# Optimization experiments

Hardware: AMD Instinct MI355X
Metric: run time of the kernel (lower is better)

Reference implementation:

```python
import jax, jax.numpy as jnp
import numpy as np

EPS = 1e-12  # matches tf l2_normalize epsilon behavior closely enough for testing

def setup_inputs() -> dict:
    key = jax.random.key(0)
    k1, k2 = jax.random.split(key)
    B, M, D = 512, 65536, 512
    context = jax.random.normal(k1, (B, D), dtype=jnp.float32)
    memory = jax.random.normal(k2, (M, D), dtype=jnp.float32)
    return {"context": context, "memory": memory}

def reference(context, memory):
    # tf.keras.losses.cosine_similarity returns NEGATIVE cosine similarity:
    # sim[b,m] = -sum(l2norm(context[b]) * l2norm(memory[m]))
    ctx_n = context / jnp.sqrt(jnp.maximum(jnp.sum(context * context, axis=-1, keepdims=True), EPS))
    mem_n = memory / jnp.sqrt(jnp.maximum(jnp.sum(memory * memory, axis=-1, keepdims=True), EPS))
    sim = -jnp.einsum('bd,md->bm', ctx_n, mem_n)  # [B, M]
    best = jnp.argmin(sim, axis=-1)               # [B], = argmax cosine
    # recall: gather then expand_dims(axis=0) -> [1, B, D]
    return memory[best][None, :, :]
```

## Files before the change

kernel.cpp:

```cpp
#include <hip/hip_runtime.h>
#include <hip/hip_bf16.h>
#include <stdint.h>

#define D_DIM 512
#define B_CTX 512
#define M_MEM 65536
#define BM 128
#define BB 128
#define BK 32
#define GBK 64
#define LDSPAD 40
#define DELTA_COS 2.5e-3f
#define LISTCAP 2048
#define CVT_MEM_BLOCKS (M_MEM / 32)
#define CVT_BLOCKS (CVT_MEM_BLOCKS + B_CTX / 32)

typedef __attribute__((ext_vector_type(8))) short short8;
typedef __attribute__((ext_vector_type(4))) float floatx4;

__device__ __forceinline__ uint32_t f32_order(float s) {
    uint32_t u = __float_as_uint(s);
    return (u & 0x80000000u) ? ~u : (u | 0x80000000u);
}
__device__ __forceinline__ float f32_unorder(uint32_t v) {
    uint32_t u = (v & 0x80000000u) ? (v & 0x7FFFFFFFu) : ~v;
    return __uint_as_float(u);
}
__device__ __forceinline__ uint32_t pack_bf16_rtn(float a, float b) {
    uint32_t ua = __float_as_uint(a) + 0x8000u;
    uint32_t ub = __float_as_uint(b) + 0x8000u;
    return (ua >> 16) | (ub & 0xFFFF0000u);
}

typedef const __attribute__((address_space(1))) void gv_t;
typedef __attribute__((address_space(3))) void lv_t;
__device__ __forceinline__ void gload_lds16(const uint16_t* g, uint16_t* l) {
    __builtin_amdgcn_global_load_lds((gv_t*)g, (lv_t*)l, 16, 0, 0);
}

__global__ void detect_init(const uint32_t* __restrict__ mem_raw,
                            uint32_t* __restrict__ flag) {
    __shared__ int cnt;
    if (threadIdx.x == 0) cnt = 0;
    __syncthreads();
    int s = 0;
    #pragma unroll
    for (int i = 0; i < 8; ++i) {
        uint32_t u = mem_raw[threadIdx.x * 8 + i];
        uint32_t e = (u >> 7) & 0xFFu;
        s += (e >= 96u && e <= 144u) ? 1 : 0;
    }
    atomicAdd(&cnt, s);
    __syncthreads();
    if (threadIdx.x == 0) *flag = (cnt > 256) ? 1u : 0u;
}

__global__ __launch_bounds__(256) void convert_scale(const void* __restrict__ ctxv,
                                                     const void* __restrict__ memv,
                                                     const uint32_t* __restrict__ flag,
                                                     uint16_t* __restrict__ mem_s,
                                                     uint16_t* __restrict__ ctx_b) {
    const bool isbf = (*flag != 0u);
    const int lane = threadIdx.x & 63;
    const int w = threadIdx.x >> 6;
    if (blockIdx.x < CVT_MEM_BLOCKS) {
        const int gw = blockIdx.x * 4 + w;
        #pragma unroll
        for (int i = 0; i < 8; ++i) {
            const int r = gw * 8 + i;
            float x[8];
            if (isbf) {
                uint4 v = *((const uint4*)((const uint16_t*)memv + (size_t)r * D_DIM) + lane);
                uint32_t ww[4] = {v.x, v.y, v.z, v.w};
                #pragma unroll
                for (int j = 0; j < 4; ++j) {
                    x[2 * j]     = __uint_as_float(ww[j] << 16);
                    x[2 * j + 1] = __uint_as_float(ww[j] & 0xFFFF0000u);
                }
            } else {
                const float4* p = (const float4*)((const float*)memv + (size_t)r * D_DIM) + lane * 2;
                float4 a = p[0], bq = p[1];
                x[0] = a.x; x[1] = a.y; x[2] = a.z; x[3] = a.w;
                x[4] = bq.x; x[5] = bq.y; x[6] = bq.z; x[7] = bq.w;
            }
            float nsq = 0.f;
            #pragma unroll
            for (int j = 0; j < 8; ++j) nsq = fmaf(x[j], x[j], nsq);
            #pragma unroll
            for (int o = 32; o; o >>= 1) nsq += __shfl_xor(nsq, o, 64);
            const float invn = rsqrtf(fmaxf(nsq, 1e-12f));
            uint4 ov;
            ov.x = pack_bf16_rtn(x[0] * invn, x[1] * invn);
            ov.y = pack_bf16_rtn(x[2] * invn, x[3] * invn);
            ov.z = pack_bf16_rtn(x[4] * invn, x[5] * invn);
            ov.w = pack_bf16_rtn(x[6] * invn, x[7] * invn);
            *((uint4*)(mem_s + (size_t)r * D_DIM) + lane) = ov;
        }
    } else {
        const int gw = (blockIdx.x - CVT_MEM_BLOCKS) * 4 + w;
        #pragma unroll
        for (int i = 0; i < 8; ++i) {
            const int r = gw * 8 + i;
            uint4 ov;
            if (isbf) {
                ov = *((const uint4*)((const uint16_t*)ctxv + (size_t)r * D_DIM) + lane);
            } else {
                const float4* p = (const float4*)((const float*)ctxv + (size_t)r * D_DIM) + lane * 2;
                float4 a = p[0], bq = p[1];
                ov.x = pack_bf16_rtn(a.x, a.y);
                ov.y = pack_bf16_rtn(a.z, a.w);
                ov.z = pack_bf16_rtn(bq.x, bq.y);
                ov.w = pack_bf16_rtn(bq.z, bq.w);
            }
            *((uint4*)(ctx_b + (size_t)r * D_DIM) + lane) = ov;
        }
    }
}

__global__ __launch_bounds__(256) void score_mfma(const uint16_t* __restrict__ A,
                                                  const uint16_t* __restrict__ Bc,
                                                  uint32_t* __restrict__ tmax,
                                                  int coarse) {
    __shared__ __align__(16) uint16_t at[BM][GBK];
    __shared__ __align__(16) uint16_t bt[BB][GBK];
    __shared__ uint32_t s_gbest[8][BB];

    const int t    = threadIdx.x;
    const int b0   = blockIdx.x * BB;
    const int m0   = blockIdx.y * BM;
    const int lane = t & 63;
    const int w    = t >> 6;
    const int wm   = w >> 1;
    const int wb   = w & 1;
    const int quad = lane >> 4;
    const int l15  = lane & 15;
    const int srow = t >> 3;
    const int scol = (t & 7) * 8;

    floatx4 acc[4][4];
    #pragma unroll
    for (int i = 0; i < 4; ++i)
        #pragma unroll
        for (int j = 0; j < 4; ++j)
            acc[i][j] = (floatx4){0.f, 0.f, 0.f, 0.f};

    for (int k0 = 0; k0 < D_DIM; k0 += GBK) {
        __syncthreads();
        #pragma unroll
        for (int q = 0; q < 4; ++q) {
            const int r = srow + q * 32;
            gload_lds16(A  + (size_t)(m0 + r) * D_DIM + k0 + scol,
                        &at[0][0] + (size_t)(q * 256 + (w << 6)) * 8);
            gload_lds16(Bc + (size_t)(b0 + r) * D_DIM + k0 + scol,
                        &bt[0][0] + (size_t)(q * 256 + (w << 6)) * 8);
        }
        __syncthreads();
        #pragma unroll
        for (int kk = 0; kk < 2; ++kk) {
            short8 af[4], bg[4];
            #pragma unroll
            for (int i = 0; i < 4; ++i)
                af[i] = *(const short8*)&at[wm * 64 + i * 16 + l15][kk * 32 + quad * 8];
            #pragma unroll
            for (int j = 0; j < 4; ++j)
                bg[j] = *(const short8*)&bt[wb * 64 + j * 16 + l15][kk * 32 + quad * 8];
            #pragma unroll
            for (int i = 0; i < 4; ++i)
                #pragma unroll
                for (int j = 0; j < 4; ++j)
                    acc[i][j] = __builtin_amdgcn_mfma_f32_16x16x32_bf16(af[i], bg[j], acc[i][j], 0, 0, 0);
        }
    }

    #pragma unroll
    for (int i = 0; i < 4; ++i)
        #pragma unroll
        for (int j = 0; j < 4; ++j) {
            uint32_t k = 0;
            #pragma unroll
            for (int r = 0; r < 4; ++r) {
                uint32_t kk = f32_order(acc[i][j][r]);
                k = kk > k ? kk : k;
            }
            uint32_t o1 = __shfl_xor(k, 16, 64); k = o1 > k ? o1 : k;
            uint32_t o2 = __shfl_xor(k, 32, 64); k = o2 > k ? o2 : k;
            if (quad == 0) s_gbest[wm * 4 + i][wb * 64 + j * 16 + l15] = k;
        }
    __syncthreads();

    if (!coarse) {
        const int G0 = blockIdx.y * 8;
        for (int e = t; e < 8 * BB; e += 256) {
            const int col = e >> 3, g = e & 7;
            tmax[(size_t)(b0 + col) * 4096 + G0 + g] = s_gbest[g][col];
        }
    } else {
        if (t < BB) {
            uint32_t k = s_gbest[0][t];
            #pragma unroll
            for (int g = 1; g < 8; ++g) k = s_gbest[g][t] > k ? s_gbest[g][t] : k;
            tmax[(size_t)(b0 + t) * 512 + blockIdx.y] = k;
        }
    }
}

__global__ __launch_bounds__(256) void score_phase1(const void* __restrict__ ctxv,
                                                    const void* __restrict__ memv,
                                                    const uint32_t* __restrict__ flag,
                                                    uint32_t* __restrict__ tmax,
                                                    int coarse) {
    __shared__ __align__(16) uint16_t at[BM][LDSPAD];
    __shared__ __align__(16) uint16_t bt[BB][LDSPAD];
    __shared__ float s_nsq[BM];
    __shared__ uint32_t s_gbest[8][BB];

    const int t    = threadIdx.x;
    const int b0   = blockIdx.x * BB;
    const int m0   = blockIdx.y * BM;
    const int lane = t & 63;
    const int w    = t >> 6;
    const int wm   = w >> 1;
    const int wb   = w & 1;
    const int quad = lane >> 4;
    const int l15  = lane & 15;
    const int srow = t >> 2;
    const int scol = (t & 3) * 8;

    floatx4 acc[4][4];
    #pragma unroll
    for (int i = 0; i < 4; ++i)
        #pragma unroll
        for (int j = 0; j < 4; ++j)
            acc[i][j] = (floatx4){0.f, 0.f, 0.f, 0.f};

    float nsq0 = 0.f, nsq1 = 0.f;
    const bool isbf = (*flag != 0u);

    for (int k0 = 0; k0 < D_DIM; k0 += BK) {
        __syncthreads();
        if (isbf) {
            const uint16_t* mp = (const uint16_t*)memv;
            const uint16_t* cp = (const uint16_t*)ctxv;
            uint4 va0 = *(const uint4*)(mp + (size_t)(m0 + srow) * D_DIM + k0 + scol);
            uint4 va1 = *(const uint4*)(mp + (size_t)(m0 + srow + 64) * D_DIM + k0 + scol);
            uint4 vb0 = *(const uint4*)(cp + (size_t)(b0 + srow) * D_DIM + k0 + scol);
            uint4 vb1 = *(const uint4*)(cp + (size_t)(b0 + srow + 64) * D_DIM + k0 + scol);
            *(uint4*)&at[srow][scol] = va0;
            *(uint4*)&at[srow + 64][scol] = va1;
            *(uint4*)&bt[srow][scol] = vb0;
            *(uint4*)&bt[srow + 64][scol] = vb1;
            uint32_t wa0[4] = {va0.x, va0.y, va0.z, va0.w};
            uint32_t wa1[4] = {va1.x, va1.y, va1.z, va1.w};
            #pragma unroll
            for (int i = 0; i < 4; ++i) {
                float a = __uint_as_float(wa0[i] << 16);
                float b = __uint_as_float(wa0[i] & 0xFFFF0000u);
                nsq0 = fmaf(a, a, nsq0); nsq0 = fmaf(b, b, nsq0);
                float c = __uint_as_float(wa1[i] << 16);
                float d = __uint_as_float(wa1[i] & 0xFFFF0000u);
                nsq1 = fmaf(c, c, nsq1); nsq1 = fmaf(d, d, nsq1);
            }
        } else {
            const float* mp = (const float*)memv;
            const float* cp = (const float*)ctxv;
            const float4* pa0 = (const float4*)(mp + (size_t)(m0 + srow) * D_DIM + k0 + scol);
            const float4* pa1 = (const float4*)(mp + (size_t)(m0 + srow + 64) * D_DIM + k0 + scol);
            const float4* pb0 = (const float4*)(cp + (size_t)(b0 + srow) * D_DIM + k0 + scol);
            const float4* pb1 = (const float4*)(cp + (size_t)(b0 + srow + 64) * D_DIM + k0 + scol);
            float4 a0 = pa0[0], a1 = pa0[1], a2 = pa1[0], a3 = pa1[1];
            float4 c0 = pb0[0], c1 = pb0[1], c2 = pb1[0], c3 = pb1[1];
            uint4 va0 = {pack_bf16_rtn(a0.x, a0.y), pack_bf16_rtn(a0.z, a0.w),
                         pack_bf16_rtn(a1.x, a1.y), pack_bf16_rtn(a1.z, a1.w)};
            uint4 va1 = {pack_bf16_rtn(a2.x, a2.y), pack_bf16_rtn(a2.z, a2.w),
                         pack_bf16_rtn(a3.x, a3.y), pack_bf16_rtn(a3.z, a3.w)};
            uint4 vb0 = {pack_bf16_rtn(c0.x, c0.y), pack_bf16_rtn(c0.z, c0.w),
                         pack_bf16_rtn(c1.x, c1.y), pack_bf16_rtn(c1.z, c1.w)};
            uint4 vb1 = {pack_bf16_rtn(c2.x, c2.y), pack_bf16_rtn(c2.z, c2.w),
                         pack_bf16_rtn(c3.x, c3.y), pack_bf16_rtn(c3.z, c3.w)};
            *(uint4*)&at[srow][scol] = va0;
            *(uint4*)&at[srow + 64][scol] = va1;
            *(uint4*)&bt[srow][scol] = vb0;
            *(uint4*)&bt[srow + 64][scol] = vb1;
            nsq0 = fmaf(a0.x, a0.x, nsq0); nsq0 = fmaf(a0.y, a0.y, nsq0);
            nsq0 = fmaf(a0.z, a0.z, nsq0); nsq0 = fmaf(a0.w, a0.w, nsq0);
            nsq0 = fmaf(a1.x, a1.x, nsq0); nsq0 = fmaf(a1.y, a1.y, nsq0);
            nsq0 = fmaf(a1.z, a1.z, nsq0); nsq0 = fmaf(a1.w, a1.w, nsq0);
            nsq1 = fmaf(a2.x, a2.x, nsq1); nsq1 = fmaf(a2.y, a2.y, nsq1);
            nsq1 = fmaf(a2.z, a2.z, nsq1); nsq1 = fmaf(a2.w, a2.w, nsq1);
            nsq1 = fmaf(a3.x, a3.x, nsq1); nsq1 = fmaf(a3.y, a3.y, nsq1);
            nsq1 = fmaf(a3.z, a3.z, nsq1); nsq1 = fmaf(a3.w, a3.w, nsq1);
        }
        __syncthreads();

        short8 af[4], bg[4];
        #pragma unroll
        for (int i = 0; i < 4; ++i)
            af[i] = *(const short8*)&at[wm * 64 + i * 16 + l15][quad * 8];
        #pragma unroll
        for (int j = 0; j < 4; ++j)
            bg[j] = *(const short8*)&bt[wb * 64 + j * 16 + l15][quad * 8];

        #pragma unroll
        for (int i = 0; i < 4; ++i)
            #pragma unroll
            for (int j = 0; j < 4; ++j)
                acc[i][j] = __builtin_amdgcn_mfma_f32_16x16x32_bf16(af[i], bg[j], acc[i][j], 0, 0, 0);
    }

    nsq0 += __shfl_xor(nsq0, 1, 64); nsq0 += __shfl_xor(nsq0, 2, 64);
    nsq1 += __shfl_xor(nsq1, 1, 64); nsq1 += __shfl_xor(nsq1, 2, 64);
    __syncthreads();
    if ((t & 3) == 0) { s_nsq[srow] = nsq0; s_nsq[srow + 64] = nsq1; }
    __syncthreads();

    float invn[4][4];
    #pragma unroll
    for (int i = 0; i < 4; ++i)
        #pragma unroll
        for (int r = 0; r < 4; ++r)
            invn[i][r] = rsqrtf(fmaxf(s_nsq[wm * 64 + i * 16 + quad * 4 + r], 1e-12f));

    #pragma unroll
    for (int i = 0; i < 4; ++i)
        #pragma unroll
        for (int j = 0; j < 4; ++j) {
            uint32_t k = 0;
            #pragma unroll
            for (int r = 0; r < 4; ++r) {
                uint32_t kk = f32_order(acc[i][j][r] * invn[i][r]);
                k = kk > k ? kk : k;
            }
            uint32_t o1 = __shfl_xor(k, 16, 64); k = o1 > k ? o1 : k;
            uint32_t o2 = __shfl_xor(k, 32, 64); k = o2 > k ? o2 : k;
            if (quad == 0) s_gbest[wm * 4 + i][wb * 64 + j * 16 + l15] = k;
        }
    __syncthreads();

    if (!coarse) {
        const int G0 = blockIdx.y * 8;
        for (int e = t; e < 8 * BB; e += 256) {
            const int col = e >> 3, g = e & 7;
            tmax[(size_t)(b0 + col) * 4096 + G0 + g] = s_gbest[g][col];
        }
    } else {
        if (t < BB) {
            uint32_t k = s_gbest[0][t];
            #pragma unroll
            for (int g = 1; g < 8; ++g) k = s_gbest[g][t] > k ? s_gbest[g][t] : k;
            tmax[(size_t)(b0 + t) * 512 + blockIdx.y] = k;
        }
    }
}

__global__ __launch_bounds__(256) void phase2(const void* __restrict__ ctxv,
                                              const void* __restrict__ memv,
                                              const uint32_t* __restrict__ flag,
                                              const uint32_t* __restrict__ tmax,
                                              void* __restrict__ outv,
                                              int ngrp, int gshift) {
    __shared__ float s_ctx[D_DIM];
    __shared__ int s_list[LISTCAP];
    __shared__ int s_cnt;
    __shared__ uint32_t s_red[4];
    __shared__ float s_cn[4];
    __shared__ double s_d[4], s_n[4];
    __shared__ int s_m[4];
    __shared__ int s_bestm;

    const int b = blockIdx.x;
    const int t = threadIdx.x;
    const int lane = t & 63;
    const int w = t >> 6;
    const bool isbf = (*flag != 0u);
    const int gmask = (1 << gshift) - 1;

    if (t == 0) s_cnt = 0;
    if (isbf) {
        if (t < 64) {
            uint4 v = *((const uint4*)((const uint16_t*)ctxv + (size_t)b * D_DIM) + t);
            uint32_t ww[4] = {v.x, v.y, v.z, v.w};
            #pragma unroll
            for (int i = 0; i < 4; ++i) {
                s_ctx[t * 8 + 2 * i]     = __uint_as_float(ww[i] << 16);
                s_ctx[t * 8 + 2 * i + 1] = __uint_as_float(ww[i] & 0xFFFF0000u);
            }
        }
    } else {
        if (t < 128)
            ((float4*)s_ctx)[t] = ((const float4*)((const float*)ctxv + (size_t)b * D_DIM))[t];
    }
    __syncthreads();

    float cs = s_ctx[t] * s_ctx[t] + s_ctx[t + 256] * s_ctx[t + 256];
    #pragma unroll
    for (int o = 32; o; o >>= 1) cs += __shfl_xor(cs, o, 64);
    if (lane == 0) s_cn[w] = cs;

    const uint32_t* tk = tmax + (size_t)b * ngrp;
    const int nk = ngrp >> 8;
    uint32_t km = 0;
    for (int i = 0; i < nk; ++i) {
        uint32_t v = tk[t + (i << 8)];
        km = v > km ? v : km;
    }
    #pragma unroll
    for (int o = 32; o; o >>= 1) { uint32_t ot = __shfl_xor(km, o, 64); km = ot > km ? ot : km; }
    if (lane == 0) s_red[w] = km;
    __syncthreads();
    uint32_t kbest = s_red[0];
    #pragma unroll
    for (int i = 1; i < 4; ++i) kbest = s_red[i] > kbest ? s_red[i] : kbest;
    const float cnorm = sqrtf(s_cn[0] + s_cn[1] + s_cn[2] + s_cn[3]);
    const uint32_t keyT = f32_order(f32_unorder(kbest) - DELTA_COS * cnorm);

    for (int i = 0; i < nk; ++i) {
        uint32_t v = tk[t + (i << 8)];
        if (v >= keyT) {
            int idx = atomicAdd(&s_cnt, 1);
            if (idx < LISTCAP) s_list[idx] = t + (i << 8);
        }
    }
    __syncthreads();
    int cnt = s_cnt; if (cnt > LISTCAP) cnt = LISTCAP;
    const int total = cnt << gshift;

    double bd = -1.0e300, bn = 1.0;
    double bp = bd * 1.0e300;
    int bm = 0x7FFFFFFF;
    const float* cb = s_ctx + lane * 8;

    for (int base = w * 2; base < total; base += 8) {
        const bool has1 = (base + 1 < total);
        const int ia = base, ib = has1 ? base + 1 : base;
        const int ma = (s_list[ia >> gshift] << gshift) + (ia & gmask);
        const int mb = (s_list[ib >> gshift] << gshift) + (ib & gmask);
        double d0 = 0.0, n0 = 0.0, d1 = 0.0, n1 = 0.0;
        if (isbf) {
            uint4 va = *((const uint4*)((const uint16_t*)memv + (size_t)ma * D_DIM) + lane);
            uint4 vb = *((const uint4*)((const uint16_t*)memv + (size_t)mb * D_DIM) + lane);
            uint32_t wa[4] = {va.x, va.y, va.z, va.w};
            uint32_t wbv[4] = {vb.x, vb.y, vb.z, vb.w};
            #pragma unroll
            for (int i = 0; i < 4; ++i) {
                float a0 = __uint_as_float(wa[i] << 16);
                float a1 = __uint_as_float(wa[i] & 0xFFFF0000u);
                d0 += (double)a0 * (double)cb[2 * i];
                d0 += (double)a1 * (double)cb[2 * i + 1];
                n0 += (double)a0 * (double)a0 + (double)a1 * (double)a1;
                float b0v = __uint_as_float(wbv[i] << 16);
                float b1v = __uint_as_float(wbv[i] & 0xFFFF0000u);
                d1 += (double)b0v * (double)cb[2 * i];
                d1 += (double)b1v * (double)cb[2 * i + 1];
                n1 += (double)b0v * (double)b0v + (double)b1v * (double)b1v;
            }
        } else {
            const float4* pa = (const float4*)((const float*)memv + (size_t)ma * D_DIM) + lane * 2;
            const float4* pb = (const float4*)((const float*)memv + (size_t)mb * D_DIM) + lane * 2;
            float4 a0 = pa[0], a1 = pa[1], b0v = pb[0], b1v = pb[1];
            float xa[8] = {a0.x, a0.y, a0.z, a0.w, a1.x, a1.y, a1.z, a1.w};
            float xb[8] = {b0v.x, b0v.y, b0v.z, b0v.w, b1v.x, b1v.y, b1v.z, b1v.w};
            #pragma unroll
            for (int i = 0; i < 8; ++i) {
                d0 += (double)xa[i] * (double)cb[i];
                n0 += (double)xa[i] * (double)xa[i];
                d1 += (double)xb[i] * (double)cb[i];
                n1 += (double)xb[i] * (double)xb[i];
            }
        }
        #pragma unroll
        for (int o = 32; o; o >>= 1) {
            d0 += __shfl_xor(d0, o, 64);
            n0 += __shfl_xor(n0, o, 64);
            d1 += __shfl_xor(d1, o, 64);
            n1 += __shfl_xor(n1, o, 64);
        }
        double p0 = d0 * fabs(d0);
        double lhs = p0 * bn, rhs = bp * n0;
        if (lhs > rhs || (lhs == rhs && ma < bm)) { bd = d0; bn = n0; bp = p0; bm = ma; }
        if (has1) {
            double p1 = d1 * fabs(d1);
            double lhs1 = p1 * bn, rhs1 = bp * n1;
            if (lhs1 > rhs1 || (lhs1 == rhs1 && mb < bm)) { bd = d1; bn = n1; bp = p1; bm = mb; }
        }
    }
    if (lane == 0) { s_d[w] = bd; s_n[w] = bn; s_m[w] = bm; }
    __syncthreads();
    if (t == 0) {
        double cd = s_d[0], cn2 = s_n[0], cp = cd * fabs(cd);
        int cm = s_m[0];
        #pragma unroll
        for (int i = 1; i < 4; ++i) {
            double pd = s_d[i], pn = s_n[i], pp = pd * fabs(pd);
            double lhs = pp * cn2, rhs = cp * pn;
            if (lhs > rhs || (lhs == rhs && s_m[i] < cm)) { cd = pd; cn2 = pn; cp = pp; cm = s_m[i]; }
        }
        s_bestm = cm;
    }
    __syncthreads();
    const int mbest = s_bestm;
    if (isbf) {
        if (t < 64)
            ((uint4*)((uint16_t*)outv + (size_t)b * D_DIM))[t] =
                ((const uint4*)((const uint16_t*)memv + (size_t)mbest * D_DIM))[t];
    } else {
        if (t < 128)
            ((float4*)((float*)outv + (size_t)b * D_DIM))[t] =
                ((const float4*)((const float*)memv + (size_t)mbest * D_DIM))[t];
    }
}

extern "C" void kernel_launch(void* const* d_in, const int* in_sizes, int n_in,
                              void* d_out, int out_size, void* d_ws, size_t ws_size,
                              hipStream_t stream) {
    const void* ctx = d_in[0];
    const void* mem = d_in[1];
    if (in_sizes[0] > in_sizes[1]) { ctx = d_in[1]; mem = d_in[0]; }

    const size_t fineBytes   = (size_t)B_CTX * 4096 * 4;
    const size_t coarseBytes = (size_t)B_CTX * 512 * 4;
    const size_t ctxBytes    = (size_t)B_CTX * D_DIM * 2;
    const size_t memBytes    = (size_t)M_MEM * D_DIM * 2;
    const size_t fastBytes   = fineBytes + 256 + ctxBytes + memBytes;
    dim3 grid(B_CTX / BB, M_MEM / BM);

    if (ws_size >= fastBytes) {
        uint32_t* tmax  = (uint32_t*)d_ws;
        uint32_t* flag  = (uint32_t*)((char*)d_ws + fineBytes);
        uint16_t* ctx_b = (uint16_t*)((char*)d_ws + fineBytes + 256);
        uint16_t* mem_s = (uint16_t*)((char*)d_ws + fineBytes + 256 + ctxBytes);
        detect_init<<<1, 64, 0, stream>>>((const uint32_t*)mem, flag);
        convert_scale<<<CVT_BLOCKS, 256, 0, stream>>>(ctx, mem, flag, mem_s, ctx_b);
        score_mfma<<<grid, 256, 0, stream>>>(mem_s, ctx_b, tmax, 0);
        phase2<<<B_CTX, 256, 0, stream>>>(ctx, mem, flag, tmax, d_out, 4096, 4);
    } else if (ws_size >= fineBytes + 256) {
        uint32_t* tmax = (uint32_t*)d_ws;
        uint32_t* flag = (uint32_t*)((char*)d_ws + fineBytes);
        detect_init<<<1, 64, 0, stream>>>((const uint32_t*)mem, flag);
        score_phase1<<<grid, 256, 0, stream>>>(ctx, mem, flag, tmax, 0);
        phase2<<<B_CTX, 256, 0, stream>>>(ctx, mem, flag, tmax, d_out, 4096, 4);
    } else {
        uint32_t* tmax = (uint32_t*)d_ws;
        uint32_t* flag = (uint32_t*)((char*)d_ws + coarseBytes);
        detect_init<<<1, 64, 0, stream>>>((const uint32_t*)mem, flag);
        score_phase1<<<grid, 256, 0, stream>>>(ctx, mem, flag, tmax, 1);
        phase2<<<B_CTX, 256, 0, stream>>>(ctx, mem, flag, tmax, d_out, 512, 7);
    }
}
```

Baseline: 293.5 us.

## Double-buffer score_mfma LDS tiles with swizzled layout and remapped block order

```diff
diff --git a/kernel.cpp b/kernel.cpp
--- a/kernel.cpp
+++ b/kernel.cpp
@@ -8,7 +8,7 @@
 #define BM 128
 #define BB 128
 #define BK 32
-#define GBK 64
+#define GBK 32
 #define LDSPAD 40
 #define DELTA_COS 2.5e-3f
 #define LISTCAP 2048
@@ -117,25 +117,44 @@
     }
 }
 
-__global__ __launch_bounds__(256) void score_mfma(const uint16_t* __restrict__ A,
-                                                  const uint16_t* __restrict__ Bc,
-                                                  uint32_t* __restrict__ tmax,
-                                                  int coarse) {
-    __shared__ __align__(16) uint16_t at[BM][GBK];
-    __shared__ __align__(16) uint16_t bt[BB][GBK];
+#define STAGE(buf, kofs)                                                          \
+    do {                                                                          \
+        gload_lds16(ga0 + (kofs), &at[buf][0][0] + (size_t)((w << 6)) * 8);       \
+        gload_lds16(ga1 + (kofs), &at[buf][0][0] + (size_t)(256 + (w << 6)) * 8); \
+        gload_lds16(gb0 + (kofs), &bt[buf][0][0] + (size_t)((w << 6)) * 8);       \
+        gload_lds16(gb1 + (kofs), &bt[buf][0][0] + (size_t)(256 + (w << 6)) * 8); \
+    } while (0)
+
+__global__ __launch_bounds__(256, 4) void score_mfma(const uint16_t* __restrict__ A,
+                                                     const uint16_t* __restrict__ Bc,
+                                                     uint32_t* __restrict__ tmax,
+                                                     int coarse) {
+    __shared__ __align__(16) uint16_t at[2][BM][GBK];
+    __shared__ __align__(16) uint16_t bt[2][BB][GBK];
     __shared__ uint32_t s_gbest[8][BB];
 
+    const int h  = blockIdx.y * gridDim.x + blockIdx.x;
+    const int v  = (h & 7) * 256 + (h >> 3);
+    const int bxp = v & 3;
+    const int byp = v >> 2;
+
     const int t    = threadIdx.x;
-    const int b0   = blockIdx.x * BB;
-    const int m0   = blockIdx.y * BM;
+    const int b0   = bxp * BB;
+    const int m0   = byp * BM;
     const int lane = t & 63;
     const int w    = t >> 6;
     const int wm   = w >> 1;
     const int wb   = w & 1;
     const int quad = lane >> 4;
     const int l15  = lane & 15;
-    const int srow = t >> 3;
-    const int scol = (t & 7) * 8;
+    const int srow = t >> 2;
+    const int scol_sw = (((t & 3) ^ ((t >> 3) & 3)) << 3);
+    const int rc = ((quad ^ ((l15 >> 1) & 3)) << 3);
+
+    const uint16_t* ga0 = A  + (size_t)(m0 + srow) * D_DIM + scol_sw;
+    const uint16_t* ga1 = A  + (size_t)(m0 + srow + 64) * D_DIM + scol_sw;
+    const uint16_t* gb0 = Bc + (size_t)(b0 + srow) * D_DIM + scol_sw;
+    const uint16_t* gb1 = Bc + (size_t)(b0 + srow + 64) * D_DIM + scol_sw;
 
     floatx4 acc[4][4];
     #pragma unroll
@@ -144,32 +163,41 @@
         for (int j = 0; j < 4; ++j)
             acc[i][j] = (floatx4){0.f, 0.f, 0.f, 0.f};
 
-    for (int k0 = 0; k0 < D_DIM; k0 += GBK) {
+    STAGE(0, 0);
+    __syncthreads();
+
+    int cur = 0;
+    #pragma unroll
+    for (int it = 0; it < (D_DIM / GBK) - 1; ++it) {
+        STAGE(cur ^ 1, (it + 1) * GBK);
+        short8 af[4], bg[4];
+        #pragma unroll
+        for (int i = 0; i < 4; ++i)
+            af[i] = *(const short8*)&at[cur][wm * 64 + i * 16 + l15][rc];
+        #pragma unroll
+        for (int j = 0; j < 4; ++j)
+            bg[j] = *(const short8*)&bt[cur][wb * 64 + j * 16 + l15][rc];
+        #pragma unroll
+        for (int i = 0; i < 4; ++i)
+            #pragma unroll
+            for (int j = 0; j < 4; ++j)
+                acc[i][j] = __builtin_amdgcn_mfma_f32_16x16x32_bf16(af[i], bg[j], acc[i][j], 0, 0, 0);
         __syncthreads();
-        #pragma unroll
-        for (int q = 0; q < 4; ++q) {
-            const int r = srow + q * 32;
-            gload_lds16(A  + (size_t)(m0 + r) * D_DIM + k0 + scol,
-                        &at[0][0] + (size_t)(q * 256 + (w << 6)) * 8);
-            gload_lds16(Bc + (size_t)(b0 + r) * D_DIM + k0 + scol,
-                        &bt[0][0] + (size_t)(q * 256 + (w << 6)) * 8);
-        }
-        __syncthreads();
-        #pragma unroll
-        for (int kk = 0; kk < 2; ++kk) {
-            short8 af[4], bg[4];
-            #pragma unroll
-            for (int i = 0; i < 4; ++i)
-                af[i] = *(const short8*)&at[wm * 64 + i * 16 + l15][kk * 32 + quad * 8];
+        cur ^= 1;
+    }
+    {
+        short8 af[4], bg[4];
+        #pragma unroll
+        for (int i = 0; i < 4; ++i)
+            af[i] = *(const short8*)&at[cur][wm * 64 + i * 16 + l15][rc];
+        #pragma unroll
+        for (int j = 0; j < 4; ++j)
+            bg[j] = *(const short8*)&bt[cur][wb * 64 + j * 16 + l15][rc];
+        #pragma unroll
+        for (int i = 0; i < 4; ++i)
             #pragma unroll
             for (int j = 0; j < 4; ++j)
-                bg[j] = *(const short8*)&bt[wb * 64 + j * 16 + l15][kk * 32 + quad * 8];
-            #pragma unroll
-            for (int i = 0; i < 4; ++i)
-                #pragma unroll
-                for (int j = 0; j < 4; ++j)
-                    acc[i][j] = __builtin_amdgcn_mfma_f32_16x16x32_bf16(af[i], bg[j], acc[i][j], 0, 0, 0);
-        }
+                acc[i][j] = __builtin_amdgcn_mfma_f32_16x16x32_bf16(af[i], bg[j], acc[i][j], 0, 0, 0);
     }
 
     #pragma unroll
@@ -189,7 +217,7 @@
     __syncthreads();
 
     if (!coarse) {
-        const int G0 = blockIdx.y * 8;
+        const int G0 = byp * 8;
         for (int e = t; e < 8 * BB; e += 256) {
             const int col = e >> 3, g = e & 7;
             tmax[(size_t)(b0 + col) * 4096 + G0 + g] = s_gbest[g][col];
@@ -199,7 +227,7 @@
             uint32_t k = s_gbest[0][t];
             #pragma unroll
             for (int g = 1; g < 8; ++g) k = s_gbest[g][t] > k ? s_gbest[g][t] : k;
-            tmax[(size_t)(b0 + t) * 512 + blockIdx.y] = k;
+            tmax[(size_t)(b0 + t) * 512 + byp] = k;
         }
     }
 }
@@ -288,7 +316,7 @@
             nsq1 = fmaf(a2.x, a2.x, nsq1); nsq1 = fmaf(a2.y, a2.y, nsq1);
             nsq1 = fmaf(a2.z, a2.z, nsq1); nsq1 = fmaf(a2.w, a2.w, nsq1);
             nsq1 = fmaf(a3.x, a3.x, nsq1); nsq1 = fmaf(a3.y, a3.y, nsq1);
-            nsq1 = fmaf(a3.z, a3.z, nsq1); nsq1 = fmaf(a3.w, a3.w, nsq1);
+            nsq1 = fmaf(a3.w, a3.w, nsq1); nsq1 = fmaf(a3.z, a3.z, nsq1);
         }
         __syncthreads();
 
```

Result: faster. 271.2 us (-7.6%).
